# Kernel optimization log

Hardware: AMD Instinct MI355X
Metric: run time of the kernel (lower is better)

Reference implementation:

```python
import jax, jax.numpy as jnp
import numpy as np
from jax import lax


def run_gru(seq, w_ih, w_hh, b_ih, b_hh):
    """PyTorch-convention GRU. seq: (T, N, E) -> outputs (T, N, H), h0 = 0."""
    H = w_hh.shape[1]
    gx = jnp.einsum('tne,ge->tng', seq, w_ih) + b_ih  # (T, N, 3H), precomputed input gates

    def step(h, gx_t):
        gh = h @ w_hh.T + b_hh
        xr, xz, xn = jnp.split(gx_t, 3, axis=-1)
        hr, hz, hn = jnp.split(gh, 3, axis=-1)
        r = jax.nn.sigmoid(xr + hr)
        z = jax.nn.sigmoid(xz + hz)
        n = jnp.tanh(xn + r * hn)
        h_new = (1.0 - z) * n + z * h
        return h_new, h_new

    h0 = jnp.zeros((seq.shape[1], H), dtype=seq.dtype)
    _, hs = lax.scan(step, h0, gx)
    return hs


def setup_inputs() -> dict:
    key = jax.random.key(0)
    ks = jax.random.split(key, 20)
    B, T, I, E, Ha, Hb, O = 32, 64, 256, 256, 256, 256, 1
    s = 0.05
    return {
        'x': jax.random.normal(ks[0], (B, T, I), dtype=jnp.float32),
        'emb_w': jax.random.normal(ks[1], (E, I), dtype=jnp.float32) * s,
        'emb_b': jax.random.normal(ks[2], (E,), dtype=jnp.float32) * s,
        'a_wih': jax.random.normal(ks[3], (3 * Ha, E), dtype=jnp.float32) * s,
        'a_whh': jax.random.normal(ks[4], (3 * Ha, Ha), dtype=jnp.float32) * s,
        'a_bih': jax.random.normal(ks[5], (3 * Ha,), dtype=jnp.float32) * s,
        'a_bhh': jax.random.normal(ks[6], (3 * Ha,), dtype=jnp.float32) * s,
        'b_wih': jax.random.normal(ks[7], (3 * Hb, E), dtype=jnp.float32) * s,
        'b_whh': jax.random.normal(ks[8], (3 * Hb, Hb), dtype=jnp.float32) * s,
        'b_bih': jax.random.normal(ks[9], (3 * Hb,), dtype=jnp.float32) * s,
        'b_bhh': jax.random.normal(ks[10], (3 * Hb,), dtype=jnp.float32) * s,
        'alpha_w': jax.random.normal(ks[11], (1, Ha), dtype=jnp.float32) * s,
        'alpha_b': jax.random.normal(ks[12], (1,), dtype=jnp.float32) * s,
        'beta_w': jax.random.normal(ks[13], (E, Hb), dtype=jnp.float32) * s,
        'beta_b': jax.random.normal(ks[14], (E,), dtype=jnp.float32) * s,
        'out_w': jax.random.normal(ks[15], (O, E), dtype=jnp.float32) * s,
        'out_b': jax.random.normal(ks[16], (O,), dtype=jnp.float32) * s,
    }


def reference(x, emb_w, emb_b, a_wih, a_whh, a_bih, a_bhh,
              b_wih, b_whh, b_bih, b_bhh, alpha_w, alpha_b,
              beta_w, beta_b, out_w, out_b):
    B, T, I = x.shape
    P = T - 1  # prefix lengths 1..T-1
    xt = jnp.transpose(x, (1, 0, 2))               # (T, B, I) time-major
    emb = jnp.einsum('tbi,ei->tbe', xt, emb_w) + emb_b  # (T, B, E)
    E = emb.shape[-1]

    # Reversed prefix p (length t=p+1): rev[p, k] = emb[p - k] for k < t, else 0.
    idx = jnp.arange(P)[:, None] - jnp.arange(T)[None, :]   # (P, T)
    valid = idx >= 0
    idxc = jnp.clip(idx, 0)
    rev = jnp.where(valid[:, :, None, None], emb[idxc], 0.0)  # (P, T, B, E)

    seq = jnp.transpose(rev, (1, 0, 2, 3)).reshape(T, P * B, E)  # (T, P*B, E)
    ha = run_gru(seq, a_wih, a_whh, a_bih, a_bhh)  # (T, P*B, Ha)
    hb = run_gru(seq, b_wih, b_whh, b_bih, b_bhh)  # (T, P*B, Hb)
    ha = jnp.transpose(ha.reshape(T, P, B, -1), (1, 0, 2, 3))  # (P, T, B, Ha)
    hb = jnp.transpose(hb.reshape(T, P, B, -1), (1, 0, 2, 3))

    # flip back within each prefix (same index map), then * 0.5 as in the source
    rows = jnp.arange(P)[:, None]
    fa = ha[rows, idxc] * 0.5   # (P, T, B, Ha); positions >= t are junk, masked below
    fb = hb[rows, idxc] * 0.5

    pre = jnp.einsum('ptbh,h->ptb', fa, alpha_w[0]) + alpha_b[0]
    logits = jnp.where(valid[:, :, None], pre, -jnp.inf)
    alpha = jax.nn.softmax(logits, axis=1)                       # softmax over time per prefix
    beta = jnp.tanh(jnp.einsum('ptbh,eh->ptbe', fb, beta_w) + beta_b)  # (P, T, B, E)

    # context: c_t = sum_j alpha * beta * emb[:t]  (alpha is 0 outside prefix)
    c = jnp.einsum('ptb,ptbe,tbe->pbe', alpha, beta, emb)        # (P, B, E)
    pred = (c @ out_w.T + out_b)                                  # (P, B, 1)
    pred = jnp.transpose(pred, (1, 0, 2))                         # (B, P, 1)

    # contribution weights; w_emb / w_out enter via .data in torch (no grad)
    w_emb = lax.stop_gradient(emb_w)
    w_out0 = lax.stop_gradient(out_w)[0]
    e = jnp.einsum('ptbe,e,ei->ptbi', beta, w_out0, w_emb)        # (P, T, B, I)
    denom = jnp.arange(1, P + 1, dtype=x.dtype)[:, None, None]    # mean over t visits
    g = jnp.einsum('ptb,ptbi,tbi->pbi', alpha, e, xt) / denom     # (P, B, I)
    weight = jnp.transpose(g, (1, 0, 2))                          # (B, P, I)
    return pred, weight
```

## Files before the change

kernel.cpp:

```cpp
#include <hip/hip_runtime.h>
#include <math.h>

#define B_   32
#define T_   64
#define P_   63
#define E_   256

typedef _Float16 half8 __attribute__((ext_vector_type(8)));
typedef _Float16 half4 __attribute__((ext_vector_type(4)));
typedef float    f32x4 __attribute__((ext_vector_type(4)));

__device__ __forceinline__ float sigmoidf_(float x) { return 1.0f / (1.0f + __expf(-x)); }
__device__ __forceinline__ float tanhfast_(float x) { float e = __expf(2.0f*x); return 1.0f - 2.0f/(e + 1.0f); }

__device__ __forceinline__ void barrier_lds_() {
    asm volatile("" ::: "memory");
    asm volatile("s_waitcnt lgkmcnt(0)" ::: "memory");
    __builtin_amdgcn_s_barrier();
    asm volatile("" ::: "memory");
}

__global__ __launch_bounds__(64) void k_prep(
    const float* __restrict__ awhh, const float* __restrict__ bwhh,
    const float* __restrict__ awih, const float* __restrict__ bwih,
    const float* __restrict__ beta_w, const float* __restrict__ emb_w, const float* __restrict__ out_w,
    _Float16* __restrict__ wfa, _Float16* __restrict__ wfb,
    _Float16* __restrict__ wifa, _Float16* __restrict__ wifb,
    _Float16* __restrict__ bwf, _Float16* __restrict__ mf)
{
    int bid = blockIdx.x, l = threadIdx.x;
    if (bid < 1664) {
        const float* W; _Float16* dst; float scale = 1.0f; int r;
        if (bid < 384)       { W = awhh;   dst = wfa;  r = bid; }
        else if (bid < 768)  { W = bwhh;   dst = wfb;  r = bid - 384; }
        else if (bid < 1152) { W = awih;   dst = wifa; r = bid - 768; }
        else if (bid < 1536) { W = bwih;   dst = wifb; r = bid - 1152; }
        else                 { W = beta_w; dst = bwf;  r = bid - 1536; scale = 0.5f; }
        int ot = r >> 3, kc = r & 7;
        int orow = ot * 16 + (l & 15);
        int c0   = kc * 32 + (l >> 4) * 8;
        half8 v;
        #pragma unroll
        for (int j = 0; j < 8; ++j) v[j] = (_Float16)(scale * W[(size_t)orow * 256 + c0 + j]);
        *reinterpret_cast<half8*>(&dst[((size_t)r * 64 + l) * 8]) = v;
    } else {
        int r = bid - 1664;
        int ot = r >> 3, kc = r & 7;
        int i  = ot * 16 + (l & 15);
        int e0 = kc * 32 + (l >> 4) * 8;
        half8 v;
        #pragma unroll
        for (int j = 0; j < 8; ++j) v[j] = (_Float16)(out_w[e0 + j] * emb_w[(size_t)(e0 + j) * 256 + i]);
        *reinterpret_cast<half8*>(&mf[((size_t)r * 64 + l) * 8]) = v;
    }
}

__global__ __launch_bounds__(256) void k_emb(const float* __restrict__ x,
                                             const float* __restrict__ emb_w,
                                             const float* __restrict__ emb_b,
                                             const float* __restrict__ out_w,
                                             _Float16* __restrict__ embh,
                                             _Float16* __restrict__ ewh,
                                             _Float16* __restrict__ xh) {
    int r0 = blockIdx.x * 8;
    int tid = threadIdx.x;
    __shared__ float xs[8][E_];
    for (int rr = 0; rr < 8; ++rr) {
        int row = r0 + rr, t = row >> 5, b = row & 31;
        float xv = x[((size_t)b * T_ + t) * E_ + tid];
        xs[rr][tid] = xv;
        xh[((size_t)b * T_ + t) * E_ + tid] = (_Float16)xv;
    }
    __syncthreads();
    float acc[8];
    #pragma unroll
    for (int rr = 0; rr < 8; ++rr) acc[rr] = 0.f;
    const float* wr = emb_w + (size_t)tid * E_;
    for (int c = 0; c < 256; c += 4) {
        float4 wv = *reinterpret_cast<const float4*>(wr + c);
        #pragma unroll
        for (int rr = 0; rr < 8; ++rr) {
            float4 ev = *reinterpret_cast<const float4*>(&xs[rr][c]);
            acc[rr] += wv.x * ev.x + wv.y * ev.y + wv.z * ev.z + wv.w * ev.w;
        }
    }
    float eb = emb_b[tid], ow = out_w[tid];
    #pragma unroll
    for (int rr = 0; rr < 8; ++rr) {
        float v = acc[rr] + eb;
        embh[(size_t)(r0 + rr) * E_ + tid] = (_Float16)v;
        ewh[(size_t)(r0 + rr) * E_ + tid]  = (_Float16)(v * ow);
    }
}

__global__ __launch_bounds__(512, 2) void k_gates2(
    const _Float16* __restrict__ embh,
    const _Float16* __restrict__ wifa, const _Float16* __restrict__ wifb,
    const float* __restrict__ abih, const float* __restrict__ abhh,
    const float* __restrict__ bbih, const float* __restrict__ bbhh,
    _Float16* __restrict__ gpa, _Float16* __restrict__ gpb)
{
    __shared__ _Float16 esw[32 * E_];
    int bid = blockIdx.x;
    int g = bid >> 6, t = bid & 63;
    const _Float16* wif = g ? wifb : wifa;
    const float* bih = g ? bbih : abih;
    const float* bhh = g ? bbhh : abhh;
    _Float16* gp = g ? gpb : gpa;
    int tid = threadIdx.x, w = tid >> 6, l = tid & 63, lg = l >> 4, lr = l & 15;

    #pragma unroll
    for (int q = 0; q < 2; ++q) {
        int idx = q * 512 + tid;
        int b = idx >> 5, e0 = (idx & 31) * 8;
        half8 v = *reinterpret_cast<const half8*>(&embh[((size_t)t * 32 + b) * E_ + e0]);
        *reinterpret_cast<half8*>(&esw[b * E_ + (e0 ^ ((b & 7) << 3))]) = v;
    }
    half8 aw[3][2][8];
    #pragma unroll
    for (int g3 = 0; g3 < 3; ++g3)
        #pragma unroll
        for (int i = 0; i < 2; ++i)
            #pragma unroll
            for (int kc = 0; kc < 8; ++kc)
                aw[g3][i][kc] = *reinterpret_cast<const half8*>(
                    &wif[(((size_t)(g3 * 16 + 2 * w + i) * 8 + kc) * 64 + l) * 8]);
    f32x4 acc[3][2][2];
    #pragma unroll
    for (int g3 = 0; g3 < 3; ++g3)
        #pragma unroll
        for (int i = 0; i < 2; ++i)
            #pragma unroll
            for (int rt = 0; rt < 2; ++rt)
                #pragma unroll
                for (int j = 0; j < 4; ++j) {
                    int d = g3 * 256 + 32 * w + 16 * i + lg * 4 + j;
                    acc[g3][i][rt][j] = bih[d] + ((g3 < 2) ? bhh[d] : 0.f);
                }
    __syncthreads();
    #pragma unroll
    for (int kc = 0; kc < 8; ++kc) {
        half8 eb[2];
        #pragma unroll
        for (int rt = 0; rt < 2; ++rt)
            eb[rt] = *reinterpret_cast<const half8*>(
                &esw[(rt * 16 + lr) * E_ + ((kc * 32 + lg * 8) ^ ((lr & 7) << 3))]);
        #pragma unroll
        for (int g3 = 0; g3 < 3; ++g3)
            #pragma unroll
            for (int i = 0; i < 2; ++i)
                #pragma unroll
                for (int rt = 0; rt < 2; ++rt)
                    acc[g3][i][rt] = __builtin_amdgcn_mfma_f32_16x16x32_f16(
                        aw[g3][i][kc], eb[rt], acc[g3][i][rt], 0, 0, 0);
    }
    #pragma unroll
    for (int g3 = 0; g3 < 3; ++g3)
        #pragma unroll
        for (int rt = 0; rt < 2; ++rt) {
            half8 v;
            #pragma unroll
            for (int i = 0; i < 2; ++i)
                #pragma unroll
                for (int j = 0; j < 4; ++j) v[i * 4 + j] = (_Float16)acc[g3][i][rt][j];
            *reinterpret_cast<half8*>(
                &gp[((((size_t)t * 2 + rt) * 8 + w) * 3 + g3) * 512 + l * 8]) = v;
        }
}

__global__ __launch_bounds__(512, 2) __attribute__((amdgpu_waves_per_eu(2, 2))) void k_gru_f(
    const _Float16* __restrict__ gpa, const _Float16* __restrict__ gpb,
    const _Float16* __restrict__ wfa, const _Float16* __restrict__ wfb,
    const float* __restrict__ abhh, const float* __restrict__ bbhh,
    const float* __restrict__ alpha_w, const float* __restrict__ alpha_b,
    float* __restrict__ pre, _Float16* __restrict__ hstore)
{
    extern __shared__ char smem[];
    half8*    wlds = reinterpret_cast<half8*>(smem);
    _Float16* hsp  = reinterpret_cast<_Float16*>(smem + 98304);
    float*    red  = reinterpret_cast<float*>(smem + 98304 + 16384);

    int bid = blockIdx.x;
    int p   = 62 - (bid >> 2);
    int g   = (bid >> 1) & 1;
    int bh  = bid & 1;
    int tid = threadIdx.x;
    int w = tid >> 6, l = tid & 63, lg = l >> 4, lr = l & 15;
    const _Float16* gp  = g ? gpb : gpa;
    const _Float16* wf  = g ? wfb : wfa;
    const float*    bhh = g ? bbhh : abhh;

    half8 wreg[3][2][6];
    #pragma unroll
    for (int g3 = 0; g3 < 3; ++g3)
        #pragma unroll
        for (int i = 0; i < 2; ++i) {
            int ot = g3 * 16 + 2 * w + i;
            #pragma unroll
            for (int kc = 0; kc < 6; ++kc)
                wreg[g3][i][kc] = *reinterpret_cast<const half8*>(&wf[((size_t)(ot * 8 + kc) * 64 + l) * 8]);
        }
    #pragma unroll
    for (int q = 0; q < 12; ++q) {
        int idx = q * 512 + tid;
        int ot = idx >> 7, kcs = (idx >> 6) & 1, l2 = idx & 63;
        wlds[idx] = *reinterpret_cast<const half8*>(&wf[((size_t)(ot * 8 + 6 + kcs) * 64 + l2) * 8]);
    }
    float bhn[2][4], awv[2][4];
    #pragma unroll
    for (int i = 0; i < 2; ++i)
        #pragma unroll
        for (int j = 0; j < 4; ++j) {
            int d = 32 * w + 16 * i + lg * 4 + j;
            bhn[i][j] = bhh[512 + d];
            awv[i][j] = alpha_w[d];
        }
    float ab = alpha_b[0];
    float hreg[2][4];
    #pragma unroll
    for (int i = 0; i < 2; ++i)
        #pragma unroll
        for (int j = 0; j < 4; ++j) hreg[i][j] = 0.f;
    __syncthreads();

    size_t tri = (size_t)p * (p + 1) / 2;

    for (int k = 0; k <= p; ++k) {
        int t_in = p - k;
        int wr = k & 1, rb = wr ^ 1;
        if (k > 0 && g == 0 && tid < 16) {
            float s = 0.f;
            #pragma unroll
            for (int q = 0; q < 8; ++q) s += red[(rb * 16 + tid) * 8 + q];
            pre[((size_t)p * T_ + (t_in + 1)) * B_ + bh * 16 + tid] = 0.5f * s + ab;
        }
        half8 gch[3];
        {
            const _Float16* gq = gp + (((size_t)(t_in * 2 + bh) * 8 + w) * 3) * 512 + l * 8;
            #pragma unroll
            for (int c = 0; c < 3; ++c)
                gch[c] = *reinterpret_cast<const half8*>(gq + (size_t)c * 512);
        }
        f32x4 acc[3][2];
        #pragma unroll
        for (int g3 = 0; g3 < 3; ++g3)
            #pragma unroll
            for (int i = 0; i < 2; ++i)
                #pragma unroll
                for (int j = 0; j < 4; ++j) acc[g3][i][j] = 0.f;
        if (k > 0) {
            half8 bhv[2];
            {
                int cb = (lg * 8) ^ ((lr & 7) << 3);
                bhv[0] = *reinterpret_cast<const half8*>(&hsp[(rb * 16 + lr) * 256 + cb]);
            }
            #pragma unroll
            for (int kc = 0; kc < 8; ++kc) {
                if (kc < 7) {
                    int cb = ((kc + 1) * 32 + lg * 8) ^ ((lr & 7) << 3);
                    bhv[(kc + 1) & 1] = *reinterpret_cast<const half8*>(&hsp[(rb * 16 + lr) * 256 + cb]);
                }
                if (kc < 6) {
                    #pragma unroll
                    for (int g3 = 0; g3 < 3; ++g3)
                        #pragma unroll
                        for (int i = 0; i < 2; ++i)
                            acc[g3][i] = __builtin_amdgcn_mfma_f32_16x16x32_f16(
                                wreg[g3][i][kc], bhv[kc & 1], acc[g3][i], 0, 0, 0);
                } else {
                    #pragma unroll
                    for (int g3 = 0; g3 < 3; ++g3)
                        #pragma unroll
                        for (int i = 0; i < 2; ++i) {
                            half8 wlv = wlds[((g3 * 16 + 2 * w + i) * 2 + (kc - 6)) * 64 + l];
                            acc[g3][i] = __builtin_amdgcn_mfma_f32_16x16x32_f16(
                                wlv, bhv[kc & 1], acc[g3][i], 0, 0, 0);
                        }
                }
            }
        }
        _Float16* hdst = hstore + ((tri + (size_t)k) * B_ + bh * 16 + lr) * (size_t)E_ + 32 * w + lg * 4;
        #pragma unroll
        for (int i = 0; i < 2; ++i) {
            half4 hh;
            #pragma unroll
            for (int j = 0; j < 4; ++j) {
                int e = i * 4 + j;
                float rg = sigmoidf_(acc[0][i][j] + (float)gch[0][e]);
                float zg = sigmoidf_(acc[1][i][j] + (float)gch[1][e]);
                float ng = tanhfast_((float)gch[2][e] + rg * (acc[2][i][j] + bhn[i][j]));
                float h  = (1.f - zg) * ng + zg * hreg[i][j];
                hreg[i][j] = h;
                hh[j] = (_Float16)h;
            }
            int ce = (32 * w + 16 * i + lg * 4) ^ ((lr & 7) << 3);
            *reinterpret_cast<half4*>(&hsp[(wr * 16 + lr) * 256 + ce]) = hh;
            if (g) *reinterpret_cast<half4*>(hdst + 16 * i) = hh;
        }
        if (!g) {
            float pa = 0.f;
            #pragma unroll
            for (int i = 0; i < 2; ++i)
                #pragma unroll
                for (int j = 0; j < 4; ++j) pa += hreg[i][j] * awv[i][j];
            pa += __shfl_xor(pa, 16, 64);
            pa += __shfl_xor(pa, 32, 64);
            if (l < 16) red[(wr * 16 + l) * 8 + w] = pa;
        }
        barrier_lds_();
    }
    if (g == 0 && tid < 16) {
        int wl = p & 1;
        float s = 0.f;
        #pragma unroll
        for (int q = 0; q < 8; ++q) s += red[(wl * 16 + tid) * 8 + q];
        pre[((size_t)p * T_ + 0) * B_ + bh * 16 + tid] = 0.5f * s + ab;
    }
}

__global__ __launch_bounds__(512, 2) void k_att3(
    const _Float16* __restrict__ hH,
    const _Float16* __restrict__ bwf, const _Float16* __restrict__ mf,
    const float* __restrict__ beta_b,
    const float* __restrict__ pre,
    const _Float16* __restrict__ ewh, const _Float16* __restrict__ xh,
    const float* __restrict__ out_b,
    float* __restrict__ out)
{
    extern __shared__ char smem[];
    _Float16* hs   = reinterpret_cast<_Float16*>(smem);
    _Float16* es2  = reinterpret_cast<_Float16*>(smem + 32768);
    _Float16* xs2  = reinterpret_cast<_Float16*>(smem + 65536);
    float*    alds = reinterpret_cast<float*>(smem + 98304);
    float*    red2 = reinterpret_cast<float*>(smem + 98304 + 256);
    int tid = threadIdx.x, w = tid >> 6, l = tid & 63, lg = l >> 4, lr = l & 15;

    half8 aw2[2][8], am2[2][8];
    #pragma unroll
    for (int i = 0; i < 2; ++i)
        #pragma unroll
        for (int kc = 0; kc < 8; ++kc) {
            size_t fo = (((size_t)(2 * w + i) * 8 + kc) * 64 + l) * 8;
            aw2[i][kc] = *reinterpret_cast<const half8*>(&bwf[fo]);
            am2[i][kc] = *reinterpret_cast<const half8*>(&mf[fo]);
        }
    float bb2[2][4];
    #pragma unroll
    for (int i = 0; i < 2; ++i)
        #pragma unroll
        for (int j = 0; j < 4; ++j)
            bb2[i][j] = beta_b[(2 * w + i) * 16 + lg * 4 + j];
    float ob = out_b[0];

    for (int it = 0; it < 8; ++it) {
        int pair = blockIdx.x * 8 + it;
        int p = pair >> 5, b = pair & 31;
        size_t tri = (size_t)p * (p + 1) / 2;
        #pragma unroll
        for (int q = 0; q < 4; ++q) {
            int idx = q * 512 + tid;
            int k = idx >> 5, e0 = (idx & 31) * 8;
            int sw = e0 ^ ((k & 7) << 3);
            half8 hv, ev;
            if (k <= p) {
                hv = *reinterpret_cast<const half8*>(&hH[((tri + (size_t)(p - k)) * B_ + b) * 256 + e0]);
                ev = *reinterpret_cast<const half8*>(&ewh[((size_t)k * B_ + b) * 256 + e0]);
            } else {
                #pragma unroll
                for (int j = 0; j < 8; ++j) { hv[j] = (_Float16)0.f; ev[j] = (_Float16)0.f; }
            }
            *reinterpret_cast<half8*>(&hs[k * 256 + sw])  = hv;
            *reinterpret_cast<half8*>(&es2[k * 256 + sw]) = ev;
            *reinterpret_cast<half8*>(&xs2[k * 256 + sw]) =
                *reinterpret_cast<const half8*>(&xh[((size_t)b * T_ + k) * 256 + e0]);
        }
        if (tid < 64) {
            float v = (tid <= p) ? pre[((size_t)p * T_ + tid) * B_ + b] : -3.4e38f;
            float m = v;
            #pragma unroll
            for (int off = 32; off > 0; off >>= 1) m = fmaxf(m, __shfl_xor(m, off, 64));
            float e = (tid <= p) ? __expf(v - m) : 0.f;
            float s = e;
            #pragma unroll
            for (int off = 32; off > 0; off >>= 1) s += __shfl_xor(s, off, 64);
            alds[tid] = e / s;
        }
        __syncthreads();
        f32x4 acc2[2][4];
        #pragma unroll
        for (int i = 0; i < 2; ++i)
            #pragma unroll
            for (int rt = 0; rt < 4; ++rt)
                #pragma unroll
                for (int j = 0; j < 4; ++j) acc2[i][rt][j] = bb2[i][j];
        #pragma unroll
        for (int kc = 0; kc < 8; ++kc) {
            half8 hb[4];
            #pragma unroll
            for (int rt = 0; rt < 4; ++rt)
                hb[rt] = *reinterpret_cast<const half8*>(&hs[(rt * 16 + lr) * 256 + ((kc * 32 + lg * 8) ^ ((lr & 7) << 3))]);
            #pragma unroll
            for (int i = 0; i < 2; ++i)
                #pragma unroll
                for (int rt = 0; rt < 4; ++rt)
                    acc2[i][rt] = __builtin_amdgcn_mfma_f32_16x16x32_f16(aw2[i][kc], hb[rt], acc2[i][rt], 0, 0, 0);
        }
        float pv = 0.f;
        half4 ureg[2][4];
        #pragma unroll
        for (int i = 0; i < 2; ++i)
            #pragma unroll
            for (int rt = 0; rt < 4; ++rt) {
                int k = rt * 16 + lr;
                float al = alds[k];
                int d0 = (2 * w + i) * 16 + lg * 4;
                half4 ev4 = *reinterpret_cast<const half4*>(&es2[k * 256 + (d0 ^ ((lr & 7) << 3))]);
                #pragma unroll
                for (int j = 0; j < 4; ++j) {
                    float u = al * tanhfast_(acc2[i][rt][j]);
                    ureg[i][rt][j] = (_Float16)u;
                    pv += u * (float)ev4[j];
                }
            }
        __syncthreads();
        #pragma unroll
        for (int i = 0; i < 2; ++i)
            #pragma unroll
            for (int rt = 0; rt < 4; ++rt) {
                int k = rt * 16 + lr;
                int d0 = (2 * w + i) * 16 + lg * 4;
                *reinterpret_cast<half4*>(&hs[k * 256 + (d0 ^ ((lr & 7) << 3))]) = ureg[i][rt];
            }
        #pragma unroll
        for (int off = 1; off < 64; off <<= 1) pv += __shfl_xor(pv, off, 64);
        if (l == 0) red2[w] = pv;
        __syncthreads();
        if (tid == 0) {
            float s = 0.f;
            #pragma unroll
            for (int q = 0; q < 8; ++q) s += red2[q];
            out[(size_t)b * P_ + p] = s + ob;
        }
        f32x4 a2[2][4];
        #pragma unroll
        for (int i = 0; i < 2; ++i)
            #pragma unroll
            for (int rt = 0; rt < 4; ++rt)
                #pragma unroll
                for (int j = 0; j < 4; ++j) a2[i][rt][j] = 0.f;
        #pragma unroll
        for (int kc = 0; kc < 8; ++kc) {
            half8 ub[4];
            #pragma unroll
            for (int rt = 0; rt < 4; ++rt)
                ub[rt] = *reinterpret_cast<const half8*>(&hs[(rt * 16 + lr) * 256 + ((kc * 32 + lg * 8) ^ ((lr & 7) << 3))]);
            #pragma unroll
            for (int i = 0; i < 2; ++i)
                #pragma unroll
                for (int rt = 0; rt < 4; ++rt)
                    a2[i][rt] = __builtin_amdgcn_mfma_f32_16x16x32_f16(am2[i][kc], ub[rt], a2[i][rt], 0, 0, 0);
        }
        float r4[2][4];
        #pragma unroll
        for (int i = 0; i < 2; ++i)
            #pragma unroll
            for (int j = 0; j < 4; ++j) r4[i][j] = 0.f;
        #pragma unroll
        for (int i = 0; i < 2; ++i)
            #pragma unroll
            for (int rt = 0; rt < 4; ++rt) {
                int k = rt * 16 + lr;
                int i0 = (2 * w + i) * 16 + lg * 4;
                half4 xv4 = *reinterpret_cast<const half4*>(&xs2[k * 256 + (i0 ^ ((lr & 7) << 3))]);
                #pragma unroll
                for (int j = 0; j < 4; ++j) r4[i][j] += a2[i][rt][j] * (float)xv4[j];
            }
        #pragma unroll
        for (int off = 1; off < 16; off <<= 1)
            #pragma unroll
            for (int i = 0; i < 2; ++i)
                #pragma unroll
                for (int j = 0; j < 4; ++j) r4[i][j] += __shfl_xor(r4[i][j], off, 64);
        if (lr == 0) {
            float inv = 1.f / (float)(p + 1);
            #pragma unroll
            for (int i = 0; i < 2; ++i) {
                f32x4 v;
                #pragma unroll
                for (int j = 0; j < 4; ++j) v[j] = r4[i][j] * inv;
                *reinterpret_cast<f32x4*>(&out[2016 + ((size_t)b * P_ + p) * 256 + (2 * w + i) * 16 + lg * 4]) = v;
            }
        }
        __syncthreads();
    }
}

extern "C" void kernel_launch(void* const* d_in, const int* in_sizes, int n_in,
                              void* d_out, int out_size, void* d_ws, size_t ws_size,
                              hipStream_t stream) {
    const float* x       = (const float*)d_in[0];
    const float* emb_w   = (const float*)d_in[1];
    const float* emb_b   = (const float*)d_in[2];
    const float* a_wih   = (const float*)d_in[3];
    const float* a_whh   = (const float*)d_in[4];
    const float* a_bih   = (const float*)d_in[5];
    const float* a_bhh   = (const float*)d_in[6];
    const float* b_wih   = (const float*)d_in[7];
    const float* b_whh   = (const float*)d_in[8];
    const float* b_bih   = (const float*)d_in[9];
    const float* b_bhh   = (const float*)d_in[10];
    const float* alpha_w = (const float*)d_in[11];
    const float* alpha_b = (const float*)d_in[12];
    const float* beta_w  = (const float*)d_in[13];
    const float* beta_b  = (const float*)d_in[14];
    const float* out_w   = (const float*)d_in[15];
    const float* out_b   = (const float*)d_in[16];
    float* out = (float*)d_out;

    float* ws = (float*)d_ws;
    _Float16* embh = (_Float16*)ws;
    _Float16* ewh  = embh + 524288;
    _Float16* xh   = ewh  + 524288;
    _Float16* gpa  = xh   + 524288;
    _Float16* gpb  = gpa  + 1572864;
    float* pre     = (float*)(gpb + 1572864);
    _Float16* wfa  = (_Float16*)(pre + 129024);
    _Float16* wfb  = wfa + 196608;
    _Float16* wifa = wfb + 196608;
    _Float16* wifb = wifa + 196608;
    _Float16* bwf  = wifb + 196608;
    _Float16* mf   = bwf + 65536;
    _Float16* hH   = mf  + 65536;

    const int GRU_LDS = 98304 + 16384 + 1024;
    (void)hipFuncSetAttribute((const void*)k_gru_f,
                              hipFuncAttributeMaxDynamicSharedMemorySize, GRU_LDS);
    const int ATT_LDS = 98304 + 256 + 32;
    (void)hipFuncSetAttribute((const void*)k_att3,
                              hipFuncAttributeMaxDynamicSharedMemorySize, ATT_LDS);

    k_prep<<<1792, 64, 0, stream>>>(a_whh, b_whh, a_wih, b_wih, beta_w, emb_w, out_w,
                                    wfa, wfb, wifa, wifb, bwf, mf);
    k_emb<<<256, 256, 0, stream>>>(x, emb_w, emb_b, out_w, embh, ewh, xh);
    k_gates2<<<128, 512, 0, stream>>>(embh, wifa, wifb, a_bih, a_bhh, b_bih, b_bhh, gpa, gpb);
    k_gru_f<<<252, 512, GRU_LDS, stream>>>(gpa, gpb, wfa, wfb, a_bhh, b_bhh,
                                           alpha_w, alpha_b, pre, hH);
    k_att3<<<252, 512, ATT_LDS, stream>>>(hH, bwf, mf, beta_b, pre, ewh, xh, out_b, out);
}
```

Baseline: 287.2 us.

## Split GRU recurrence across 16 waves with one output tile per wave

Doubles the GRU recurrence block from 512 to 1024 threads so each wave handles one 16-row output tile per gate instead of two. The gate precompute layout changes to match, and the alpha reduction now sums over 16 wave partials. The goal is to shorten the serial per-step critical path by halving the MFMA chain and elementwise work per wave. The cost is more waves contending at the per-step barrier and at the LDS reads of h and the weights.

```diff
diff --git a/kernel.cpp b/kernel.cpp
--- a/kernel.cpp
+++ b/kernel.cpp
@@ -157,18 +157,18 @@
     #pragma unroll
     for (int g3 = 0; g3 < 3; ++g3)
         #pragma unroll
-        for (int rt = 0; rt < 2; ++rt) {
-            half8 v;
-            #pragma unroll
-            for (int i = 0; i < 2; ++i)
-                #pragma unroll
-                for (int j = 0; j < 4; ++j) v[i * 4 + j] = (_Float16)acc[g3][i][rt][j];
-            *reinterpret_cast<half8*>(
-                &gp[((((size_t)t * 2 + rt) * 8 + w) * 3 + g3) * 512 + l * 8]) = v;
-        }
-}
-
-__global__ __launch_bounds__(512, 2) __attribute__((amdgpu_waves_per_eu(2, 2))) void k_gru_f(
+        for (int rt = 0; rt < 2; ++rt)
+            #pragma unroll
+            for (int i = 0; i < 2; ++i) {
+                half4 v;
+                #pragma unroll
+                for (int j = 0; j < 4; ++j) v[j] = (_Float16)acc[g3][i][rt][j];
+                *reinterpret_cast<half4*>(
+                    &gp[((((size_t)t * 2 + rt) * 16 + (2 * w + i)) * 3 + g3) * 256 + l * 4]) = v;
+            }
+}
+
+__global__ __launch_bounds__(1024, 4) void k_gru_f(
     const _Float16* __restrict__ gpa, const _Float16* __restrict__ gpb,
     const _Float16* __restrict__ wfa, const _Float16* __restrict__ wfb,
     const float* __restrict__ abhh, const float* __restrict__ bbhh,
@@ -190,37 +190,31 @@
     const _Float16* wf  = g ? wfb : wfa;
     const float*    bhh = g ? bbhh : abhh;
 
-    half8 wreg[3][2][6];
-    #pragma unroll
-    for (int g3 = 0; g3 < 3; ++g3)
-        #pragma unroll
-        for (int i = 0; i < 2; ++i) {
-            int ot = g3 * 16 + 2 * w + i;
-            #pragma unroll
-            for (int kc = 0; kc < 6; ++kc)
-                wreg[g3][i][kc] = *reinterpret_cast<const half8*>(&wf[((size_t)(ot * 8 + kc) * 64 + l) * 8]);
-        }
-    #pragma unroll
-    for (int q = 0; q < 12; ++q) {
-        int idx = q * 512 + tid;
+    half8 wreg[3][6];
+    #pragma unroll
+    for (int g3 = 0; g3 < 3; ++g3) {
+        int ot = g3 * 16 + w;
+        #pragma unroll
+        for (int kc = 0; kc < 6; ++kc)
+            wreg[g3][kc] = *reinterpret_cast<const half8*>(&wf[((size_t)(ot * 8 + kc) * 64 + l) * 8]);
+    }
+    #pragma unroll
+    for (int q = 0; q < 6; ++q) {
+        int idx = q * 1024 + tid;
         int ot = idx >> 7, kcs = (idx >> 6) & 1, l2 = idx & 63;
         wlds[idx] = *reinterpret_cast<const half8*>(&wf[((size_t)(ot * 8 + 6 + kcs) * 64 + l2) * 8]);
     }
-    float bhn[2][4], awv[2][4];
-    #pragma unroll
-    for (int i = 0; i < 2; ++i)
-        #pragma unroll
-        for (int j = 0; j < 4; ++j) {
-            int d = 32 * w + 16 * i + lg * 4 + j;
-            bhn[i][j] = bhh[512 + d];
-            awv[i][j] = alpha_w[d];
-        }
+    float bhn[4], awv[4];
+    #pragma unroll
+    for (int j = 0; j < 4; ++j) {
+        int d = 16 * w + lg * 4 + j;
+        bhn[j] = bhh[512 + d];
+        awv[j] = alpha_w[d];
+    }
     float ab = alpha_b[0];
-    float hreg[2][4];
-    #pragma unroll
-    for (int i = 0; i < 2; ++i)
-        #pragma unroll
-        for (int j = 0; j < 4; ++j) hreg[i][j] = 0.f;
+    float hreg[4];
+    #pragma unroll
+    for (int j = 0; j < 4; ++j) hreg[j] = 0.f;
     __syncthreads();
 
     size_t tri = (size_t)p * (p + 1) / 2;
@@ -231,23 +225,21 @@
         if (k > 0 && g == 0 && tid < 16) {
             float s = 0.f;
             #pragma unroll
-            for (int q = 0; q < 8; ++q) s += red[(rb * 16 + tid) * 8 + q];
+            for (int q = 0; q < 16; ++q) s += red[(rb * 16 + tid) * 16 + q];
             pre[((size_t)p * T_ + (t_in + 1)) * B_ + bh * 16 + tid] = 0.5f * s + ab;
         }
-        half8 gch[3];
+        half4 gch[3];
         {
-            const _Float16* gq = gp + (((size_t)(t_in * 2 + bh) * 8 + w) * 3) * 512 + l * 8;
+            const _Float16* gq = gp + (((size_t)(t_in * 2 + bh) * 16 + w) * 3) * 256 + l * 4;
             #pragma unroll
             for (int c = 0; c < 3; ++c)
-                gch[c] = *reinterpret_cast<const half8*>(gq + (size_t)c * 512);
-        }
-        f32x4 acc[3][2];
+                gch[c] = *reinterpret_cast<const half4*>(gq + (size_t)c * 256);
+        }
+        f32x4 acc[3];
         #pragma unroll
         for (int g3 = 0; g3 < 3; ++g3)
             #pragma unroll
-            for (int i = 0; i < 2; ++i)
-                #pragma unroll
-                for (int j = 0; j < 4; ++j) acc[g3][i][j] = 0.f;
+            for (int j = 0; j < 4; ++j) acc[g3][j] = 0.f;
         if (k > 0) {
             half8 bhv[2];
             {
@@ -263,49 +255,42 @@
                 if (kc < 6) {
                     #pragma unroll
                     for (int g3 = 0; g3 < 3; ++g3)
-                        #pragma unroll
-                        for (int i = 0; i < 2; ++i)
-                            acc[g3][i] = __builtin_amdgcn_mfma_f32_16x16x32_f16(
-                                wreg[g3][i][kc], bhv[kc & 1], acc[g3][i], 0, 0, 0);
+                        acc[g3] = __builtin_amdgcn_mfma_f32_16x16x32_f16(
+                            wreg[g3][kc], bhv[kc & 1], acc[g3], 0, 0, 0);
                 } else {
                     #pragma unroll
-                    for (int g3 = 0; g3 < 3; ++g3)
-                        #pragma unroll
-                        for (int i = 0; i < 2; ++i) {
-                            half8 wlv = wlds[((g3 * 16 + 2 * w + i) * 2 + (kc - 6)) * 64 + l];
-                            acc[g3][i] = __builtin_amdgcn_mfma_f32_16x16x32_f16(
-                                wlv, bhv[kc & 1], acc[g3][i], 0, 0, 0);
-                        }
+                    for (int g3 = 0; g3 < 3; ++g3) {
+                        half8 wlv = wlds[((g3 * 16 + w) * 2 + (kc - 6)) * 64 + l];
+                        acc[g3] = __builtin_amdgcn_mfma_f32_16x16x32_f16(
+                            wlv, bhv[kc & 1], acc[g3], 0, 0, 0);
+                    }
                 }
             }
         }
-        _Float16* hdst = hstore + ((tri + (size_t)k) * B_ + bh * 16 + lr) * (size_t)E_ + 32 * w + lg * 4;
-        #pragma unroll
-        for (int i = 0; i < 2; ++i) {
-            half4 hh;
-            #pragma unroll
-            for (int j = 0; j < 4; ++j) {
-                int e = i * 4 + j;
-                float rg = sigmoidf_(acc[0][i][j] + (float)gch[0][e]);
-                float zg = sigmoidf_(acc[1][i][j] + (float)gch[1][e]);
-                float ng = tanhfast_((float)gch[2][e] + rg * (acc[2][i][j] + bhn[i][j]));
-                float h  = (1.f - zg) * ng + zg * hreg[i][j];
-                hreg[i][j] = h;
-                hh[j] = (_Float16)h;
-            }
-            int ce = (32 * w + 16 * i + lg * 4) ^ ((lr & 7) << 3);
+        half4 hh;
+        #pragma unroll
+        for (int j = 0; j < 4; ++j) {
+            float rg = sigmoidf_(acc[0][j] + (float)gch[0][j]);
+            float zg = sigmoidf_(acc[1][j] + (float)gch[1][j]);
+            float ng = tanhfast_((float)gch[2][j] + rg * (acc[2][j] + bhn[j]));
+            float h  = (1.f - zg) * ng + zg * hreg[j];
+            hreg[j] = h;
+            hh[j] = (_Float16)h;
+        }
+        {
+            int ce = (16 * w + lg * 4) ^ ((lr & 7) << 3);
             *reinterpret_cast<half4*>(&hsp[(wr * 16 + lr) * 256 + ce]) = hh;
-            if (g) *reinterpret_cast<half4*>(hdst + 16 * i) = hh;
-        }
-        if (!g) {
+        }
+        if (g) {
+            *reinterpret_cast<half4*>(
+                hstore + ((tri + (size_t)k) * B_ + bh * 16 + lr) * (size_t)E_ + 16 * w + lg * 4) = hh;
+        } else {
             float pa = 0.f;
             #pragma unroll
-            for (int i = 0; i < 2; ++i)
-                #pragma unroll
-                for (int j = 0; j < 4; ++j) pa += hreg[i][j] * awv[i][j];
+            for (int j = 0; j < 4; ++j) pa += hreg[j] * awv[j];
             pa += __shfl_xor(pa, 16, 64);
             pa += __shfl_xor(pa, 32, 64);
-            if (l < 16) red[(wr * 16 + l) * 8 + w] = pa;
+            if (l < 16) red[(wr * 16 + l) * 16 + w] = pa;
         }
         barrier_lds_();
     }
@@ -313,7 +298,7 @@
         int wl = p & 1;
         float s = 0.f;
         #pragma unroll
-        for (int q = 0; q < 8; ++q) s += red[(wl * 16 + tid) * 8 + q];
+        for (int q = 0; q < 16; ++q) s += red[(wl * 16 + tid) * 16 + q];
         pre[((size_t)p * T_ + 0) * B_ + bh * 16 + tid] = 0.5f * s + ab;
     }
 }
@@ -532,7 +517,7 @@
     _Float16* mf   = bwf + 65536;
     _Float16* hH   = mf  + 65536;
 
-    const int GRU_LDS = 98304 + 16384 + 1024;
+    const int GRU_LDS = 98304 + 16384 + 2048;
     (void)hipFuncSetAttribute((const void*)k_gru_f,
                               hipFuncAttributeMaxDynamicSharedMemorySize, GRU_LDS);
     const int ATT_LDS = 98304 + 256 + 32;
@@ -543,7 +528,7 @@
                                     wfa, wfb, wifa, wifb, bwf, mf);
     k_emb<<<256, 256, 0, stream>>>(x, emb_w, emb_b, out_w, embh, ewh, xh);
     k_gates2<<<128, 512, 0, stream>>>(embh, wifa, wifb, a_bih, a_bhh, b_bih, b_bhh, gpa, gpb);
-    k_gru_f<<<252, 512, GRU_LDS, stream>>>(gpa, gpb, wfa, wfb, a_bhh, b_bhh,
-                                           alpha_w, alpha_b, pre, hH);
+    k_gru_f<<<252, 1024, GRU_LDS, stream>>>(gpa, gpb, wfa, wfb, a_bhh, b_bhh,
+                                            alpha_w, alpha_b, pre, hH);
     k_att3<<<252, 512, ATT_LDS, stream>>>(hH, bwf, mf, beta_b, pre, ewh, xh, out_b, out);
 }
```

After: 297.4 us. 1.04x slower.
